# Optimization experiments

Measured on AMD Instinct MI355X. Metric: run time of the kernel, lower is better.

Reference implementation:

```python
import jax, jax.numpy as jnp
import numpy as np

N = 50000      # nodes
E = 800000     # edges (avg degree 16)
S = 2          # sample_size
D_IN = 128     # input_dim
D_NOISE = 64   # noise_dim
D0 = 256       # output_dims[0]
D1 = 256       # output_dims[1]


def setup_inputs() -> dict:
    key = jax.random.key(0)
    ks = jax.random.split(key, 8)
    X = jax.random.normal(ks[0], (1, N, D_IN), dtype=jnp.float32)
    edge_src = jax.random.randint(ks[1], (E,), 0, N)
    edge_dst = jax.random.randint(ks[2], (E,), 0, N)
    # Bernoulli(0.5) noise, as in torch.distributions.Bernoulli
    epsilon = (jax.random.uniform(ks[3], (S, N, D_NOISE)) < 0.5).astype(jnp.float32)
    W0 = jax.random.normal(ks[4], (D_IN + D_NOISE, D0), dtype=jnp.float32) * 0.05
    b0 = jnp.zeros((D0,), jnp.float32)
    W1 = jax.random.normal(ks[5], (D0, D1), dtype=jnp.float32) * 0.05
    b1 = jnp.zeros((D1,), jnp.float32)
    eps0 = jnp.zeros((), jnp.float32)  # GINConv learnable eps, init 0
    eps1 = jnp.zeros((), jnp.float32)
    return dict(X=X, epsilon=epsilon, edge_src=edge_src, edge_dst=edge_dst,
                W0=W0, b0=b0, W1=W1, b1=b1, eps0=eps0, eps1=eps1)


def reference(X, epsilon, edge_src, edge_dst, W0, b0, W1, b1, eps0, eps1):
    # Expand features over sample dim and concat noise: [S, N, D_IN + D_NOISE]
    feat = jnp.broadcast_to(X, (epsilon.shape[0], X.shape[1], X.shape[2]))
    h = jnp.concatenate([feat, epsilon], axis=2)

    def gin_layer(h, eps, W, b):
        # sum aggregation over in-edges: agg[:, d] += h[:, s] for each edge (s, d)
        agg = jnp.zeros_like(h).at[:, edge_dst, :].add(h[:, edge_src, :])
        return jax.nn.relu(((1.0 + eps) * h + agg) @ W + b)

    h = gin_layer(h, eps0, W0, b0)
    h = gin_layer(h, eps1, W1, b1)
    out = jax.nn.relu(h)  # outer activation applied once more in forward()
    return out, epsilon
```

## Files before the change

kernel.cpp:

```cpp
#include <hip/hip_runtime.h>
#include <hip/hip_bf16.h>

#define NN 50000
#define NE 800000
#define NS 2
#define DIN 128
#define DNOISE 64
#define DH0 192
#define DOUT 256
#define NB 49

typedef __bf16 bf16x8 __attribute__((ext_vector_type(8)));
typedef float floatx4 __attribute__((ext_vector_type(4)));


__device__ inline float bflo(unsigned int u) { return __uint_as_float(u << 16); }
__device__ inline float bfhi(unsigned int u) { return __uint_as_float(u & 0xffff0000u); }
__device__ inline unsigned short f2bf_bits(float x) {
    __hip_bfloat16 b = __float2bfloat16(x);
    return *reinterpret_cast<unsigned short*>(&b);
}
__device__ inline unsigned int pack2(float lo, float hi) {
    return (unsigned int)f2bf_bits(lo) | ((unsigned int)f2bf_bits(hi) << 16);
}


__global__ void count_kernel(const int* __restrict__ dst, int* __restrict__ cnt) {
    int i = blockIdx.x * blockDim.x + threadIdx.x;
    if (i < NE) atomicAdd(&cnt[dst[i]], 1);
}

__global__ __launch_bounds__(1024) void scanA_kernel(const int* __restrict__ cnt, int* __restrict__ bsum) {
    int i = blockIdx.x * 1024 + threadIdx.x;
    int v = (i < NN) ? cnt[i] : 0;
    for (int off = 32; off > 0; off >>= 1) v += __shfl_down(v, off);
    __shared__ int wsum[16];
    if ((threadIdx.x & 63) == 0) wsum[threadIdx.x >> 6] = v;
    __syncthreads();
    if (threadIdx.x == 0) {
        int s = 0;
        for (int k = 0; k < 16; ++k) s += wsum[k];
        bsum[blockIdx.x] = s;
    }
}

__global__ __launch_bounds__(64) void scanB_kernel(int* __restrict__ bsum) {
    int lane = threadIdx.x;
    int orig = (lane < NB) ? bsum[lane] : 0;
    int v = orig;
    for (int off = 1; off < 64; off <<= 1) {
        int t = __shfl_up(v, off);
        if (lane >= off) v += t;
    }
    if (lane < NB) bsum[lane] = v - orig;
}

__global__ __launch_bounds__(1024) void scanC_kernel(int* __restrict__ cnt, const int* __restrict__ bsum,
                                                     int* __restrict__ row_ptr) {
    __shared__ int buf[1024];
    int tid = threadIdx.x;
    int i = blockIdx.x * 1024 + tid;
    int v = (i < NN) ? cnt[i] : 0;
    buf[tid] = v;
    __syncthreads();
    for (int off = 1; off < 1024; off <<= 1) {
        int t = (tid >= off) ? buf[tid - off] : 0;
        __syncthreads();
        buf[tid] += t;
        __syncthreads();
    }
    int excl = buf[tid] - v + bsum[blockIdx.x];
    if (i < NN) { row_ptr[i + 1] = excl + v; cnt[i] = excl; }
    if (i == 0) row_ptr[0] = 0;
}

__global__ void fill_kernel(const int* __restrict__ src, const int* __restrict__ dst,
                            int* __restrict__ cursor, int* __restrict__ col_idx) {
    int i = blockIdx.x * blockDim.x + threadIdx.x;
    if (i < NE) {
        int p = atomicAdd(&cursor[dst[i]], 1);
        col_idx[p] = src[i];
    }
}

#define XQ (NN * DIN / 4)
#define XB4 ((XQ + 255) / 256)
#define NR_BLOCKS ((NS * NN + 255) / 256)

__global__ void prep_kernel(const float* __restrict__ X, unsigned short* __restrict__ Xb,
                            const float* __restrict__ noise, uint2* __restrict__ Nbit,
                            float* __restrict__ out_eps) {
    int b = blockIdx.x;
    if (b < XB4) {
        int i = b * 256 + threadIdx.x;
        if (i < XQ) {
            float4 v = reinterpret_cast<const float4*>(X)[i];
            ushort4 o;
            o.x = f2bf_bits(v.x); o.y = f2bf_bits(v.y); o.z = f2bf_bits(v.z); o.w = f2bf_bits(v.w);
            reinterpret_cast<ushort4*>(Xb)[i] = o;
        }
    } else {
        int r = (b - XB4) * 256 + threadIdx.x;
        if (r < NS * NN) {
            const float4* p = reinterpret_cast<const float4*>(noise + (size_t)r * DNOISE);
            float4* oe = reinterpret_cast<float4*>(out_eps + (size_t)r * DNOISE);
            unsigned int lo = 0, hi = 0;
            for (int q = 0; q < 8; ++q) {
                float4 v = p[q];
                oe[q] = v;
                int base = q * 4;
                lo |= (v.x != 0.f ? 1u : 0u) << base;
                lo |= (v.y != 0.f ? 1u : 0u) << (base + 1);
                lo |= (v.z != 0.f ? 1u : 0u) << (base + 2);
                lo |= (v.w != 0.f ? 1u : 0u) << (base + 3);
            }
            for (int q = 8; q < 16; ++q) {
                float4 v = p[q];
                oe[q] = v;
                int base = q * 4 - 32;
                hi |= (v.x != 0.f ? 1u : 0u) << base;
                hi |= (v.y != 0.f ? 1u : 0u) << (base + 1);
                hi |= (v.z != 0.f ? 1u : 0u) << (base + 2);
                hi |= (v.w != 0.f ? 1u : 0u) << (base + 3);
            }
            uint2 o; o.x = lo; o.y = hi;
            Nbit[r] = o;
        }
    }
}


template <int K>
__global__ void pack_w(const float* __restrict__ W, uint4* __restrict__ Wp) {
    const int n = blockIdx.x;
    const int tj = threadIdx.x;
    if (tj < K / 8) {
        unsigned short h[8];
#pragma unroll
        for (int r = 0; r < 8; ++r)
            h[r] = f2bf_bits(W[(size_t)(tj * 8 + r) * DOUT + n]);
        uint4 o;
        o.x = (unsigned)h[0] | ((unsigned)h[1] << 16);
        o.y = (unsigned)h[2] | ((unsigned)h[3] << 16);
        o.z = (unsigned)h[4] | ((unsigned)h[5] << 16);
        o.w = (unsigned)h[6] | ((unsigned)h[7] << 16);
        Wp[(size_t)((n >> 6) * (K / 8) + tj) * 64 + (n & 63)] = o;
    }
}


__global__ __launch_bounds__(256) void agg0_kernel(
    const unsigned int* __restrict__ Xb,
    const uint2* __restrict__ Nbit,
    const int* __restrict__ row_ptr, const int* __restrict__ col_idx,
    const float* __restrict__ eps0p,
    unsigned int* __restrict__ z0) {
    const int d = blockIdx.x * 2 + (threadIdx.x >> 7);
    const int cc = threadIdx.x & 127;
    const float c = 1.f + eps0p[0];
    const int beg = row_ptr[d], end = row_ptr[d + 1];
    if (cc < 64) {
        const unsigned int* src = Xb + cc;
        unsigned int u = src[(size_t)d * 64];
        float aL = c * bflo(u), aH = c * bfhi(u);
        int e = beg;
        for (; e + 3 < end; e += 4) {
            int i0 = col_idx[e], i1 = col_idx[e + 1], i2 = col_idx[e + 2], i3 = col_idx[e + 3];
            unsigned int u0 = src[(size_t)i0 * 64], u1 = src[(size_t)i1 * 64];
            unsigned int u2 = src[(size_t)i2 * 64], u3 = src[(size_t)i3 * 64];
            aL += (bflo(u0) + bflo(u1)) + (bflo(u2) + bflo(u3));
            aH += (bfhi(u0) + bfhi(u1)) + (bfhi(u2) + bfhi(u3));
        }
        for (; e < end; ++e) {
            unsigned int ue = src[(size_t)col_idx[e] * 64];
            aL += bflo(ue); aH += bfhi(ue);
        }
        unsigned int r = pack2(aL, aH);
        z0[(size_t)d * 96 + cc] = r;
        z0[(size_t)(NN + d) * 96 + cc] = r;
    } else {
        int j = cc - 64;
        int s = j >> 5, col = j & 31;
        const uint2* src = Nbit + (size_t)s * NN;
        const int word = col >> 4;
        const int sh = (2 * col) & 31;
        uint2 uS = src[d];
        unsigned int wS = word ? uS.y : uS.x;
        int c0 = 0, c1 = 0;
        int e = beg;
        for (; e + 3 < end; e += 4) {
            uint2 u0 = src[col_idx[e]], u1 = src[col_idx[e + 1]];
            uint2 u2 = src[col_idx[e + 2]], u3 = src[col_idx[e + 3]];
            unsigned int w0 = word ? u0.y : u0.x, w1 = word ? u1.y : u1.x;
            unsigned int w2 = word ? u2.y : u2.x, w3 = word ? u3.y : u3.x;
            c0 += (int)((w0 >> sh) & 1) + (int)((w1 >> sh) & 1) + (int)((w2 >> sh) & 1) + (int)((w3 >> sh) & 1);
            c1 += (int)((w0 >> (sh + 1)) & 1) + (int)((w1 >> (sh + 1)) & 1) +
                  (int)((w2 >> (sh + 1)) & 1) + (int)((w3 >> (sh + 1)) & 1);
        }
        for (; e < end; ++e) {
            uint2 ue = src[col_idx[e]];
            unsigned int we = word ? ue.y : ue.x;
            c0 += (int)((we >> sh) & 1);
            c1 += (int)((we >> (sh + 1)) & 1);
        }
        float aL = c * (float)((wS >> sh) & 1) + (float)c0;
        float aH = c * (float)((wS >> (sh + 1)) & 1) + (float)c1;
        z0[(size_t)(s * NN + d) * 96 + 64 + col] = pack2(aL, aH);
    }
}


template <bool NT>
__device__ inline void st_out(float* C, size_t idx, float v) {
    if (NT) __builtin_nontemporal_store(v, C + idx); else C[idx] = v;
}
template <bool NT>
__device__ inline void st_out(__hip_bfloat16* C, size_t idx, float v) { C[idx] = __float2bfloat16(v); }

#define GEMM_GRID 3128

template <int K, bool NT, typename OUT_T>
__global__ __launch_bounds__(256, 4) void gemm_bias_relu(
    const __hip_bfloat16* __restrict__ A, const uint4* __restrict__ Wp,
    const float* __restrict__ bias, OUT_T* __restrict__ C, int M) {
    constexpr int NJ = K / 8;
    __shared__ uint4 lds[NJ * 64];

    const int p = blockIdx.x;
    const int l = (p & 7) * (GEMM_GRID / 8) + (p >> 3);
    const int cg = l & 3;
    const int rg = l >> 2;
    const int blockRow = rg * 128;

    const int tid = threadIdx.x;
    const uint4* wsrc = Wp + (size_t)cg * (NJ * 64);
#pragma unroll
    for (int i = 0; i < NJ / 4; ++i)
        lds[i * 256 + tid] = wsrc[i * 256 + tid];
    __syncthreads();

    const int lane = tid & 63, wave = tid >> 6;
    const int lo = lane & 15, quad = lane >> 4;
    const int rowBase = blockRow + wave * 32;

    floatx4 acc[2][4];
#pragma unroll
    for (int i = 0; i < 2; ++i)
#pragma unroll
        for (int j = 0; j < 4; ++j) acc[i][j] = (floatx4){0.f, 0.f, 0.f, 0.f};

    unsigned int aoff[2];
#pragma unroll
    for (int rt = 0; rt < 2; ++rt) {
        int rowi = rowBase + rt * 16 + lo;
        if (rowi >= M) rowi = M - 1;
        aoff[rt] = (unsigned int)rowi * (unsigned int)(K * 2);
    }
    const char* Ab = (const char*)A + quad * 16;

#pragma unroll
    for (int ks = 0; ks < K / 32; ++ks) {
        bf16x8 a[2], b[4];
#pragma unroll
        for (int rt = 0; rt < 2; ++rt)
            a[rt] = *(const bf16x8*)(Ab + aoff[rt] + ks * 64);
#pragma unroll
        for (int ct = 0; ct < 4; ++ct)
            b[ct] = *(const bf16x8*)&lds[(ks * 4 + quad) * 64 + ct * 16 + lo];
#pragma unroll
        for (int rt = 0; rt < 2; ++rt)
#pragma unroll
            for (int ct = 0; ct < 4; ++ct)
                acc[rt][ct] = __builtin_amdgcn_mfma_f32_16x16x32_bf16(a[rt], b[ct], acc[rt][ct], 0, 0, 0);
    }

#pragma unroll
    for (int ct = 0; ct < 4; ++ct) {
        const int col = cg * 64 + ct * 16 + lo;
        const float bv = bias[col];
#pragma unroll
        for (int rt = 0; rt < 2; ++rt) {
#pragma unroll
            for (int r = 0; r < 4; ++r) {
                int row = rowBase + rt * 16 + quad * 4 + r;
                if (row < M) {
                    float v = acc[rt][ct][r] + bv;
                    st_out<NT>(C, (size_t)row * DOUT + col, v > 0.f ? v : 0.f);
                }
            }
        }
    }
}


__global__ __launch_bounds__(256, 6) void fused1_kernel(
    const uint2* __restrict__ h,
    const int* __restrict__ row_ptr, const int* __restrict__ col_idx,
    const float* __restrict__ eps1p,
    const uint4* __restrict__ Wp,
    const float* __restrict__ bias,
    float* __restrict__ out) {
    __shared__ uint2 zt[32 * 64];
    const int n0 = blockIdx.x * 16;
    const int tid = threadIdx.x;
    const float c = 1.f + eps1p[0];

    for (int jj = 0; jj < 8; ++jj) {
        const int d = n0 + jj * 2 + (tid >> 7);
        const int nloc = d - n0;
        const int s = (tid >> 6) & 1;
        const int cc = tid & 63;
        const int beg = row_ptr[d], end = row_ptr[d + 1];
        const uint2* src = h + (size_t)s * NN * 64 + cc;
        uint2 u = src[(size_t)d * 64];
        float aL0 = c * bflo(u.x), aH0 = c * bfhi(u.x);
        float aL1 = c * bflo(u.y), aH1 = c * bfhi(u.y);
        int e = beg;
        for (; e + 7 < end; e += 8) {
            uint2 g[8];
#pragma unroll
            for (int q = 0; q < 8; ++q) g[q] = src[(size_t)col_idx[e + q] * 64];
#pragma unroll
            for (int q = 0; q < 8; ++q) {
                aL0 += bflo(g[q].x); aH0 += bfhi(g[q].x);
                aL1 += bflo(g[q].y); aH1 += bfhi(g[q].y);
            }
        }
        for (; e + 3 < end; e += 4) {
            uint2 u0 = src[(size_t)col_idx[e] * 64], u1 = src[(size_t)col_idx[e + 1] * 64];
            uint2 u2 = src[(size_t)col_idx[e + 2] * 64], u3 = src[(size_t)col_idx[e + 3] * 64];
            aL0 += (bflo(u0.x) + bflo(u1.x)) + (bflo(u2.x) + bflo(u3.x));
            aH0 += (bfhi(u0.x) + bfhi(u1.x)) + (bfhi(u2.x) + bfhi(u3.x));
            aL1 += (bflo(u0.y) + bflo(u1.y)) + (bflo(u2.y) + bflo(u3.y));
            aH1 += (bfhi(u0.y) + bfhi(u1.y)) + (bfhi(u2.y) + bfhi(u3.y));
        }
        for (; e < end; ++e) {
            uint2 ue = src[(size_t)col_idx[e] * 64];
            aL0 += bflo(ue.x); aH0 += bfhi(ue.x);
            aL1 += bflo(ue.y); aH1 += bfhi(ue.y);
        }
        uint2 r; r.x = pack2(aL0, aH0); r.y = pack2(aL1, aH1);
        const int lr = s * 16 + nloc;
        zt[lr * 64 + (((cc >> 1) ^ (lr & 7)) << 1) + (cc & 1)] = r;
    }
    __syncthreads();

    const int lane = tid & 63, w = tid >> 6;
    const int lo = lane & 15, quad = lane >> 4;
    const int rw = w >> 1, ch = w & 1;
    const int lrow = rw * 16 + lo;

    floatx4 acc[8];
#pragma unroll
    for (int t = 0; t < 8; ++t) acc[t] = (floatx4){0.f, 0.f, 0.f, 0.f};

    const uint4* zt4 = (const uint4*)zt;
#pragma unroll
    for (int ks = 0; ks < 8; ++ks) {
        bf16x8 a = *(const bf16x8*)&zt4[lrow * 32 + ((ks * 4 + quad) ^ (lrow & 7))];
#pragma unroll
        for (int ct = 0; ct < 8; ++ct) {
            bf16x8 b = *(const bf16x8*)&Wp[(size_t)((ch * 2 + (ct >> 2)) * 32 + ks * 4 + quad) * 64 + (ct & 3) * 16 + lo];
            acc[ct] = __builtin_amdgcn_mfma_f32_16x16x32_bf16(a, b, acc[ct], 0, 0, 0);
        }
    }

#pragma unroll
    for (int ct = 0; ct < 8; ++ct) {
        const int col = ch * 128 + ct * 16 + lo;
        const float bv = bias[col];
#pragma unroll
        for (int r = 0; r < 4; ++r) {
            const int mrow = rw * 16 + quad * 4 + r;
            const int grow = (mrow >> 4) * NN + n0 + (mrow & 15);
            float v = acc[ct][r] + bv;
            __builtin_nontemporal_store(v > 0.f ? v : 0.f, out + (size_t)grow * DOUT + col);
        }
    }
}

#define FUSED1_GRID (NN / 16)

extern "C" void kernel_launch(void* const* d_in, const int* in_sizes, int n_in,
                              void* d_out, int out_size, void* d_ws, size_t ws_size,
                              hipStream_t stream) {
    const float* X = (const float*)d_in[0];
    const float* noise = (const float*)d_in[1];
    const int* esrc = (const int*)d_in[2];
    const int* edst = (const int*)d_in[3];
    const float* W0 = (const float*)d_in[4];
    const float* b0 = (const float*)d_in[5];
    const float* W1 = (const float*)d_in[6];
    const float* b1 = (const float*)d_in[7];
    const float* eps0 = (const float*)d_in[8];
    const float* eps1 = (const float*)d_in[9];
    float* out = (float*)d_out;

    const int M = NS * NN;

    char* w = (char*)d_ws;
    auto carve = [&](size_t bytes) { char* p = w; w += (bytes + 511) & ~(size_t)511; return p; };
    int* cursor = (int*)carve((size_t)NN * 4);
    int* row_ptr = (int*)carve((size_t)(NN + 1) * 4);
    int* col_idx = (int*)carve((size_t)NE * 4);
    int* bsum = (int*)carve((size_t)NB * 4);
    uint2* Nbit = (uint2*)carve((size_t)M * 8);
    uint4* Wp0 = (uint4*)carve((size_t)DH0 * DOUT * 2);
    uint4* Wp1 = (uint4*)carve((size_t)DOUT * DOUT * 2);
    char* zreg = carve((size_t)M * DOUT * 2);

    unsigned int* z0 = (unsigned int*)d_out;
    unsigned short* Xb = (unsigned short*)(zreg + (size_t)M * 96 * 4);
    __hip_bfloat16* h1 = (__hip_bfloat16*)zreg;

    hipMemsetAsync(cursor, 0, (size_t)NN * 4, stream);
    count_kernel<<<(NE + 255) / 256, 256, 0, stream>>>(edst, cursor);
    scanA_kernel<<<NB, 1024, 0, stream>>>(cursor, bsum);
    scanB_kernel<<<1, 64, 0, stream>>>(bsum);
    scanC_kernel<<<NB, 1024, 0, stream>>>(cursor, bsum, row_ptr);
    fill_kernel<<<(NE + 255) / 256, 256, 0, stream>>>(esrc, edst, cursor, col_idx);
    prep_kernel<<<XB4 + NR_BLOCKS, 256, 0, stream>>>(X, Xb, noise, Nbit,
                                                     out + (size_t)M * DOUT);
    pack_w<DH0><<<DOUT, 64, 0, stream>>>(W0, Wp0);
    pack_w<DOUT><<<DOUT, 64, 0, stream>>>(W1, Wp1);

    agg0_kernel<<<NN / 2, 256, 0, stream>>>(
        (const unsigned int*)Xb, Nbit, row_ptr, col_idx, eps0, z0);
    gemm_bias_relu<DH0, false, __hip_bfloat16><<<GEMM_GRID, 256, 0, stream>>>(
        (const __hip_bfloat16*)z0, Wp0, b0, h1, M);
    fused1_kernel<<<FUSED1_GRID, 256, 0, stream>>>(
        (const uint2*)h1, row_ptr, col_idx, eps1, Wp1, b1, out);
}
```

Before: 571.4 us.

## Fuse layer-0 aggregation with its GEMM via swizzled LDS tile

Merges the layer-0 neighbor aggregation and the bias+ReLU GEMM into one kernel. Each block aggregates 16 nodes for both samples into a swizzled shared-memory tile and runs MFMA on it directly, so the global z0 intermediate is never written or re-read. The two weight-packing launches are also merged into one. The trade-off is that B operands now come straight from global/L2 rather than LDS, and per-block GEMM reuse is lower.

```diff
diff --git a/kernel.cpp b/kernel.cpp
--- a/kernel.cpp
+++ b/kernel.cpp
@@ -130,9 +130,13 @@
 }
 
 
-template <int K>
-__global__ void pack_w(const float* __restrict__ W, uint4* __restrict__ Wp) {
-    const int n = blockIdx.x;
+__global__ void pack_both(const float* __restrict__ W0, const float* __restrict__ W1,
+                          uint4* __restrict__ Wp0, uint4* __restrict__ Wp1) {
+    const bool second = blockIdx.x >= DOUT;
+    const int n = second ? blockIdx.x - DOUT : blockIdx.x;
+    const int K = second ? DOUT : DH0;
+    const float* W = second ? W1 : W0;
+    uint4* Wp = second ? Wp1 : Wp0;
     const int tj = threadIdx.x;
     if (tj < K / 8) {
         unsigned short h[8];
@@ -149,148 +153,113 @@
 }
 
 
-__global__ __launch_bounds__(256) void agg0_kernel(
+__global__ __launch_bounds__(256, 6) void fused0_kernel(
     const unsigned int* __restrict__ Xb,
     const uint2* __restrict__ Nbit,
     const int* __restrict__ row_ptr, const int* __restrict__ col_idx,
     const float* __restrict__ eps0p,
-    unsigned int* __restrict__ z0) {
-    const int d = blockIdx.x * 2 + (threadIdx.x >> 7);
-    const int cc = threadIdx.x & 127;
+    const uint4* __restrict__ Wp,
+    const float* __restrict__ bias,
+    __hip_bfloat16* __restrict__ H) {
+    __shared__ unsigned int zt[32 * 96];
+    const int n0 = blockIdx.x * 16;
+    const int tid = threadIdx.x;
     const float c = 1.f + eps0p[0];
-    const int beg = row_ptr[d], end = row_ptr[d + 1];
-    if (cc < 64) {
-        const unsigned int* src = Xb + cc;
-        unsigned int u = src[(size_t)d * 64];
-        float aL = c * bflo(u), aH = c * bfhi(u);
-        int e = beg;
-        for (; e + 3 < end; e += 4) {
-            int i0 = col_idx[e], i1 = col_idx[e + 1], i2 = col_idx[e + 2], i3 = col_idx[e + 3];
-            unsigned int u0 = src[(size_t)i0 * 64], u1 = src[(size_t)i1 * 64];
-            unsigned int u2 = src[(size_t)i2 * 64], u3 = src[(size_t)i3 * 64];
-            aL += (bflo(u0) + bflo(u1)) + (bflo(u2) + bflo(u3));
-            aH += (bfhi(u0) + bfhi(u1)) + (bfhi(u2) + bfhi(u3));
-        }
-        for (; e < end; ++e) {
-            unsigned int ue = src[(size_t)col_idx[e] * 64];
-            aL += bflo(ue); aH += bfhi(ue);
-        }
-        unsigned int r = pack2(aL, aH);
-        z0[(size_t)d * 96 + cc] = r;
-        z0[(size_t)(NN + d) * 96 + cc] = r;
-    } else {
-        int j = cc - 64;
-        int s = j >> 5, col = j & 31;
-        const uint2* src = Nbit + (size_t)s * NN;
-        const int word = col >> 4;
-        const int sh = (2 * col) & 31;
-        uint2 uS = src[d];
-        unsigned int wS = word ? uS.y : uS.x;
-        int c0 = 0, c1 = 0;
-        int e = beg;
-        for (; e + 3 < end; e += 4) {
-            uint2 u0 = src[col_idx[e]], u1 = src[col_idx[e + 1]];
-            uint2 u2 = src[col_idx[e + 2]], u3 = src[col_idx[e + 3]];
-            unsigned int w0 = word ? u0.y : u0.x, w1 = word ? u1.y : u1.x;
-            unsigned int w2 = word ? u2.y : u2.x, w3 = word ? u3.y : u3.x;
-            c0 += (int)((w0 >> sh) & 1) + (int)((w1 >> sh) & 1) + (int)((w2 >> sh) & 1) + (int)((w3 >> sh) & 1);
-            c1 += (int)((w0 >> (sh + 1)) & 1) + (int)((w1 >> (sh + 1)) & 1) +
-                  (int)((w2 >> (sh + 1)) & 1) + (int)((w3 >> (sh + 1)) & 1);
-        }
-        for (; e < end; ++e) {
-            uint2 ue = src[col_idx[e]];
-            unsigned int we = word ? ue.y : ue.x;
-            c0 += (int)((we >> sh) & 1);
-            c1 += (int)((we >> (sh + 1)) & 1);
-        }
-        float aL = c * (float)((wS >> sh) & 1) + (float)c0;
-        float aH = c * (float)((wS >> (sh + 1)) & 1) + (float)c1;
-        z0[(size_t)(s * NN + d) * 96 + 64 + col] = pack2(aL, aH);
-    }
-}
-
-
-template <bool NT>
-__device__ inline void st_out(float* C, size_t idx, float v) {
-    if (NT) __builtin_nontemporal_store(v, C + idx); else C[idx] = v;
-}
-template <bool NT>
-__device__ inline void st_out(__hip_bfloat16* C, size_t idx, float v) { C[idx] = __float2bfloat16(v); }
-
-#define GEMM_GRID 3128
-
-template <int K, bool NT, typename OUT_T>
-__global__ __launch_bounds__(256, 4) void gemm_bias_relu(
-    const __hip_bfloat16* __restrict__ A, const uint4* __restrict__ Wp,
-    const float* __restrict__ bias, OUT_T* __restrict__ C, int M) {
-    constexpr int NJ = K / 8;
-    __shared__ uint4 lds[NJ * 64];
-
-    const int p = blockIdx.x;
-    const int l = (p & 7) * (GEMM_GRID / 8) + (p >> 3);
-    const int cg = l & 3;
-    const int rg = l >> 2;
-    const int blockRow = rg * 128;
-
-    const int tid = threadIdx.x;
-    const uint4* wsrc = Wp + (size_t)cg * (NJ * 64);
-#pragma unroll
-    for (int i = 0; i < NJ / 4; ++i)
-        lds[i * 256 + tid] = wsrc[i * 256 + tid];
+
+    for (int jj = 0; jj < 8; ++jj) {
+        const int d = n0 + jj * 2 + (tid >> 7);
+        const int nloc = d - n0;
+        const int cc = tid & 127;
+        const int beg = row_ptr[d], end = row_ptr[d + 1];
+        if (cc < 64) {
+            const unsigned int* src = Xb + cc;
+            unsigned int u = src[(size_t)d * 64];
+            float aL = c * bflo(u), aH = c * bfhi(u);
+            int e = beg;
+            for (; e + 3 < end; e += 4) {
+                int i0 = col_idx[e], i1 = col_idx[e + 1], i2 = col_idx[e + 2], i3 = col_idx[e + 3];
+                unsigned int u0 = src[(size_t)i0 * 64], u1 = src[(size_t)i1 * 64];
+                unsigned int u2 = src[(size_t)i2 * 64], u3 = src[(size_t)i3 * 64];
+                aL += (bflo(u0) + bflo(u1)) + (bflo(u2) + bflo(u3));
+                aH += (bfhi(u0) + bfhi(u1)) + (bfhi(u2) + bfhi(u3));
+            }
+            for (; e < end; ++e) {
+                unsigned int ue = src[(size_t)col_idx[e] * 64];
+                aL += bflo(ue); aH += bfhi(ue);
+            }
+            unsigned int r = pack2(aL, aH);
+            const int sw = (((cc >> 2) ^ (nloc & 7)) << 2) + (cc & 3);
+            zt[nloc * 96 + sw] = r;
+            zt[(16 + nloc) * 96 + sw] = r;
+        } else {
+            int j = cc - 64;
+            int s = j >> 5, col = j & 31;
+            const uint2* src = Nbit + (size_t)s * NN;
+            const int word = col >> 4;
+            const int sh = (2 * col) & 31;
+            uint2 uS = src[d];
+            unsigned int wS = word ? uS.y : uS.x;
+            int c0 = 0, c1 = 0;
+            int e = beg;
+            for (; e + 3 < end; e += 4) {
+                uint2 u0 = src[col_idx[e]], u1 = src[col_idx[e + 1]];
+                uint2 u2 = src[col_idx[e + 2]], u3 = src[col_idx[e + 3]];
+                unsigned int w0 = word ? u0.y : u0.x, w1 = word ? u1.y : u1.x;
+                unsigned int w2 = word ? u2.y : u2.x, w3 = word ? u3.y : u3.x;
+                c0 += (int)((w0 >> sh) & 1) + (int)((w1 >> sh) & 1) + (int)((w2 >> sh) & 1) + (int)((w3 >> sh) & 1);
+                c1 += (int)((w0 >> (sh + 1)) & 1) + (int)((w1 >> (sh + 1)) & 1) +
+                      (int)((w2 >> (sh + 1)) & 1) + (int)((w3 >> (sh + 1)) & 1);
+            }
+            for (; e < end; ++e) {
+                uint2 ue = src[col_idx[e]];
+                unsigned int we = word ? ue.y : ue.x;
+                c0 += (int)((we >> sh) & 1);
+                c1 += (int)((we >> (sh + 1)) & 1);
+            }
+            float aL = c * (float)((wS >> sh) & 1) + (float)c0;
+            float aH = c * (float)((wS >> (sh + 1)) & 1) + (float)c1;
+            const int lr = s * 16 + nloc;
+            const int ui = 64 + col;
+            zt[lr * 96 + ((((ui >> 2) ^ (lr & 7)) << 2)) + (ui & 3)] = pack2(aL, aH);
+        }
+    }
     __syncthreads();
 
-    const int lane = tid & 63, wave = tid >> 6;
+    const int lane = tid & 63, w = tid >> 6;
     const int lo = lane & 15, quad = lane >> 4;
-    const int rowBase = blockRow + wave * 32;
-
-    floatx4 acc[2][4];
-#pragma unroll
-    for (int i = 0; i < 2; ++i)
-#pragma unroll
-        for (int j = 0; j < 4; ++j) acc[i][j] = (floatx4){0.f, 0.f, 0.f, 0.f};
-
-    unsigned int aoff[2];
-#pragma unroll
-    for (int rt = 0; rt < 2; ++rt) {
-        int rowi = rowBase + rt * 16 + lo;
-        if (rowi >= M) rowi = M - 1;
-        aoff[rt] = (unsigned int)rowi * (unsigned int)(K * 2);
-    }
-    const char* Ab = (const char*)A + quad * 16;
-
-#pragma unroll
-    for (int ks = 0; ks < K / 32; ++ks) {
-        bf16x8 a[2], b[4];
-#pragma unroll
-        for (int rt = 0; rt < 2; ++rt)
-            a[rt] = *(const bf16x8*)(Ab + aoff[rt] + ks * 64);
-#pragma unroll
-        for (int ct = 0; ct < 4; ++ct)
-            b[ct] = *(const bf16x8*)&lds[(ks * 4 + quad) * 64 + ct * 16 + lo];
-#pragma unroll
-        for (int rt = 0; rt < 2; ++rt)
-#pragma unroll
-            for (int ct = 0; ct < 4; ++ct)
-                acc[rt][ct] = __builtin_amdgcn_mfma_f32_16x16x32_bf16(a[rt], b[ct], acc[rt][ct], 0, 0, 0);
-    }
-
-#pragma unroll
-    for (int ct = 0; ct < 4; ++ct) {
-        const int col = cg * 64 + ct * 16 + lo;
+    const int rw = w >> 1, ch = w & 1;
+    const int lrow = rw * 16 + lo;
+
+    floatx4 acc[8];
+#pragma unroll
+    for (int t = 0; t < 8; ++t) acc[t] = (floatx4){0.f, 0.f, 0.f, 0.f};
+
+    const uint4* zt4 = (const uint4*)zt;
+#pragma unroll
+    for (int ks = 0; ks < 6; ++ks) {
+        bf16x8 a = *(const bf16x8*)&zt4[lrow * 24 + ((ks * 4 + quad) ^ (lrow & 7))];
+#pragma unroll
+        for (int ct = 0; ct < 8; ++ct) {
+            bf16x8 b = *(const bf16x8*)&Wp[(size_t)((ch * 2 + (ct >> 2)) * 24 + ks * 4 + quad) * 64 + (ct & 3) * 16 + lo];
+            acc[ct] = __builtin_amdgcn_mfma_f32_16x16x32_bf16(a, b, acc[ct], 0, 0, 0);
+        }
+    }
+
+#pragma unroll
+    for (int ct = 0; ct < 8; ++ct) {
+        const int col = ch * 128 + ct * 16 + lo;
         const float bv = bias[col];
 #pragma unroll
-        for (int rt = 0; rt < 2; ++rt) {
-#pragma unroll
-            for (int r = 0; r < 4; ++r) {
-                int row = rowBase + rt * 16 + quad * 4 + r;
-                if (row < M) {
-                    float v = acc[rt][ct][r] + bv;
-                    st_out<NT>(C, (size_t)row * DOUT + col, v > 0.f ? v : 0.f);
-                }
-            }
-        }
-    }
-}
+        for (int r = 0; r < 4; ++r) {
+            const int mrow = rw * 16 + quad * 4 + r;
+            const int grow = (mrow >> 4) * NN + n0 + (mrow & 15);
+            float v = acc[ct][r] + bv;
+            H[(size_t)grow * DOUT + col] = __float2bfloat16(v > 0.f ? v : 0.f);
+        }
+    }
+}
+
+#define FUSED0_GRID (NN / 16)
 
 
 __global__ __launch_bounds__(256, 6) void fused1_kernel(
@@ -409,8 +378,7 @@
     uint4* Wp1 = (uint4*)carve((size_t)DOUT * DOUT * 2);
     char* zreg = carve((size_t)M * DOUT * 2);
 
-    unsigned int* z0 = (unsigned int*)d_out;
-    unsigned short* Xb = (unsigned short*)(zreg + (size_t)M * 96 * 4);
+    unsigned short* Xb = (unsigned short*)d_out;
     __hip_bfloat16* h1 = (__hip_bfloat16*)zreg;
 
     hipMemsetAsync(cursor, 0, (size_t)NN * 4, stream);
@@ -421,13 +389,10 @@
     fill_kernel<<<(NE + 255) / 256, 256, 0, stream>>>(esrc, edst, cursor, col_idx);
     prep_kernel<<<XB4 + NR_BLOCKS, 256, 0, stream>>>(X, Xb, noise, Nbit,
                                                      out + (size_t)M * DOUT);
-    pack_w<DH0><<<DOUT, 64, 0, stream>>>(W0, Wp0);
-    pack_w<DOUT><<<DOUT, 64, 0, stream>>>(W1, Wp1);
-
-    agg0_kernel<<<NN / 2, 256, 0, stream>>>(
-        (const unsigned int*)Xb, Nbit, row_ptr, col_idx, eps0, z0);
-    gemm_bias_relu<DH0, false, __hip_bfloat16><<<GEMM_GRID, 256, 0, stream>>>(
-        (const __hip_bfloat16*)z0, Wp0, b0, h1, M);
+    pack_both<<<2 * DOUT, 64, 0, stream>>>(W0, W1, Wp0, Wp1);
+
+    fused0_kernel<<<FUSED0_GRID, 256, 0, stream>>>(
+        (const unsigned int*)Xb, Nbit, row_ptr, col_idx, eps0, Wp0, b0, h1);
     fused1_kernel<<<FUSED1_GRID, 256, 0, stream>>>(
         (const uint2*)h1, row_ptr, col_idx, eps1, Wp1, b1, out);
 }
```

Result: no change. 577.5 us (+1.1%).
